# Kernel tuning notes

Measured on AMD Instinct MI355X. Metric: run time of the kernel, lower is better.

## Reference

```python
import jax, jax.numpy as jnp
import numpy as np

N = 8192
D_IN = 512
D_OUT = 256
ALPHA = 0.2
NEG = -9e15


def setup_inputs() -> dict:
    key = jax.random.key(0)
    k1, k2, k3, k4 = jax.random.split(key, 4)
    node = jax.random.normal(k1, (N, D_IN), dtype=jnp.float32)
    adj = jax.random.randint(k2, (N, N), 0, 2, dtype=jnp.int32)
    # xavier_uniform with gain=1.414
    gain = 1.414
    lim_w = gain * np.sqrt(6.0 / (D_IN + D_OUT))
    weight = jax.random.uniform(k3, (D_IN, D_OUT), minval=-lim_w, maxval=lim_w, dtype=jnp.float32)
    lim_a = gain * np.sqrt(6.0 / (2 * D_OUT + 1))
    a = jax.random.uniform(k4, (2 * D_OUT, 1), minval=-lim_a, maxval=lim_a, dtype=jnp.float32)
    bias = jnp.zeros((D_OUT,), dtype=jnp.float32)
    return {"node": node, "adj": adj, "weight": weight, "a": a, "bias": bias}


def reference(node, adj, weight, a, bias):
    # v: [N, D_OUT]
    v = node @ weight
    # per-node attention scalars: Q, K are [N, 1]
    Q = v @ a[:D_OUT, :]
    K = v @ a[D_OUT:, :]
    e = jax.nn.leaky_relu(Q + K.T, negative_slope=ALPHA)  # [N, N]
    attention = jnp.where(adj > 0, e, NEG)
    attention = jax.nn.softmax(attention, axis=1)
    # dropout is identity in eval mode (self.training == False)
    out = attention @ v  # [N, D_OUT]
    out = jax.nn.leaky_relu(out, negative_slope=ALPHA)
    # F.normalize(p=2, dim=1): x / max(||x||_2, 1e-12)
    norm = jnp.linalg.norm(out, axis=1, keepdims=True)
    out = out / jnp.maximum(norm, 1e-12)
    return out + bias
```

## Files before the change

### kernel.cpp

```cpp
#include <hip/hip_runtime.h>
#include <hip/hip_bf16.h>

#define N_NODES 8192
#define DIN     512
#define DOUT    256
#define ALPHA   0.2f
#define LOG2E   1.4426950408889634f

typedef __bf16 bf16x8 __attribute__((ext_vector_type(8)));
typedef __bf16 bf16x4 __attribute__((ext_vector_type(4)));
typedef float  f32x4  __attribute__((ext_vector_type(4)));
typedef int    i32x4  __attribute__((ext_vector_type(4)));
typedef unsigned u32x4 __attribute__((ext_vector_type(4)));

__global__ __launch_bounds__(256) void k_repack_w(const float* __restrict__ w,
                                                  bf16x8* __restrict__ wB,
                                                  unsigned* __restrict__ kmaxkey) {
    if (blockIdx.x == 0 && threadIdx.x == 0) *kmaxkey = 0u;
    int u = blockIdx.x * 256 + threadIdx.x;
    int lane = u & 63, t = u >> 6;
    int nt = t & 15, kt = t >> 4;
    int k0 = kt * 32 + (lane >> 4) * 8;
    int col = nt * 16 + (lane & 15);
    bf16x8 r;
#pragma unroll
    for (int i = 0; i < 8; ++i) r[i] = (__bf16)w[(size_t)(k0 + i) * DOUT + col];
    wB[u] = r;
}

__global__ __launch_bounds__(256) void k_gemm1f(const float* __restrict__ node,
                                                const bf16x8* __restrict__ wB,
                                                const float* __restrict__ a,
                                                bf16x8* __restrict__ vBo,
                                                float* __restrict__ Q, float* __restrict__ K,
                                                unsigned* __restrict__ kmaxkey) {
    __shared__ __bf16 vsh[32][260];
    __shared__ float qksh[32][2];
    int lane = threadIdx.x & 63, w = threadIdx.x >> 6;
    int r15 = lane & 15, g = lane >> 4;
    int nh = w & 1, rh = w >> 1;
    int rowbase = blockIdx.x * 32;
    int myrow = rowbase + rh * 16 + r15;
    const float* np = node + (size_t)myrow * DIN + g * 8;

    f32x4 acc[8];
#pragma unroll
    for (int j = 0; j < 8; ++j) acc[j] = (f32x4){0.f, 0.f, 0.f, 0.f};

    f32x4 c0 = *(const f32x4*)np;
    f32x4 c1 = *(const f32x4*)(np + 4);
    f32x4 c2 = *(const f32x4*)(np + 32);
    f32x4 c3 = *(const f32x4*)(np + 36);
    const bf16x8* wp = wB + (size_t)(nh * 8) * 64 + lane;
    bf16x8 fr0 = wp[0], fr1 = wp[64], fr2 = wp[128], fr3 = wp[192];
    bf16x8 fr4 = wp[256], fr5 = wp[320], fr6 = wp[384], fr7 = wp[448];

    for (int kt = 0; kt < 16; ++kt) {
        f32x4 u0 = c0, u1 = c1;
        c0 = c2; c1 = c3;
        if (kt + 2 < 16) {
            c2 = *(const f32x4*)(np + (kt + 2) * 32);
            c3 = *(const f32x4*)(np + (kt + 2) * 32 + 4);
        }
        bf16x8 f0 = fr0, f1 = fr1, f2 = fr2, f3 = fr3;
        bf16x8 f4 = fr4, f5 = fr5, f6 = fr6, f7 = fr7;
        if (kt + 1 < 16) {
            const bf16x8* wn = wB + ((size_t)(kt + 1) * 16 + nh * 8) * 64 + lane;
            fr0 = wn[0]; fr1 = wn[64]; fr2 = wn[128]; fr3 = wn[192];
            fr4 = wn[256]; fr5 = wn[320]; fr6 = wn[384]; fr7 = wn[448];
        }
        bf16x8 af;
#pragma unroll
        for (int i = 0; i < 4; ++i) { af[i] = (__bf16)u0[i]; af[i + 4] = (__bf16)u1[i]; }
        acc[0] = __builtin_amdgcn_mfma_f32_16x16x32_bf16(af, f0, acc[0], 0, 0, 0);
        acc[1] = __builtin_amdgcn_mfma_f32_16x16x32_bf16(af, f1, acc[1], 0, 0, 0);
        acc[2] = __builtin_amdgcn_mfma_f32_16x16x32_bf16(af, f2, acc[2], 0, 0, 0);
        acc[3] = __builtin_amdgcn_mfma_f32_16x16x32_bf16(af, f3, acc[3], 0, 0, 0);
        acc[4] = __builtin_amdgcn_mfma_f32_16x16x32_bf16(af, f4, acc[4], 0, 0, 0);
        acc[5] = __builtin_amdgcn_mfma_f32_16x16x32_bf16(af, f5, acc[5], 0, 0, 0);
        acc[6] = __builtin_amdgcn_mfma_f32_16x16x32_bf16(af, f6, acc[6], 0, 0, 0);
        acc[7] = __builtin_amdgcn_mfma_f32_16x16x32_bf16(af, f7, acc[7], 0, 0, 0);
    }

    float qp0 = 0.f, qp1 = 0.f, qp2 = 0.f, qp3 = 0.f;
    float kp0 = 0.f, kp1 = 0.f, kp2 = 0.f, kp3 = 0.f;
#pragma unroll
    for (int j = 0; j < 8; ++j) {
        int col = (nh * 8 + j) * 16 + r15;
        float a1 = a[col], a2 = a[DOUT + col];
        qp0 += acc[j][0] * a1; qp1 += acc[j][1] * a1;
        qp2 += acc[j][2] * a1; qp3 += acc[j][3] * a1;
        kp0 += acc[j][0] * a2; kp1 += acc[j][1] * a2;
        kp2 += acc[j][2] * a2; kp3 += acc[j][3] * a2;
    }
#pragma unroll
    for (int m = 1; m < 16; m <<= 1) {
        qp0 += __shfl_xor(qp0, m); qp1 += __shfl_xor(qp1, m);
        qp2 += __shfl_xor(qp2, m); qp3 += __shfl_xor(qp3, m);
        kp0 += __shfl_xor(kp0, m); kp1 += __shfl_xor(kp1, m);
        kp2 += __shfl_xor(kp2, m); kp3 += __shfl_xor(kp3, m);
    }

#pragma unroll
    for (int j = 0; j < 8; ++j)
#pragma unroll
        for (int r = 0; r < 4; ++r)
            vsh[rh * 16 + g * 4 + r][(nh * 8 + j) * 16 + r15] = (__bf16)acc[j][r];
    if (nh == 0 && r15 == 0) {
        int rl = rh * 16 + g * 4;
        qksh[rl + 0][0] = qp0; qksh[rl + 1][0] = qp1; qksh[rl + 2][0] = qp2; qksh[rl + 3][0] = qp3;
        qksh[rl + 0][1] = kp0; qksh[rl + 1][1] = kp1; qksh[rl + 2][1] = kp2; qksh[rl + 3][1] = kp3;
    }
    __syncthreads();
    if (nh == 1 && r15 == 0) {
        int rl = rh * 16 + g * 4;
        int rw = rowbase + rl;
        float q0 = qp0 + qksh[rl + 0][0], q1 = qp1 + qksh[rl + 1][0];
        float q2 = qp2 + qksh[rl + 2][0], q3 = qp3 + qksh[rl + 3][0];
        float k0 = kp0 + qksh[rl + 0][1], k1 = kp1 + qksh[rl + 1][1];
        float k2 = kp2 + qksh[rl + 2][1], k3 = kp3 + qksh[rl + 3][1];
        Q[rw + 0] = q0; Q[rw + 1] = q1; Q[rw + 2] = q2; Q[rw + 3] = q3;
        K[rw + 0] = k0; K[rw + 1] = k1; K[rw + 2] = k2; K[rw + 3] = k3;
        float km = fmaxf(fmaxf(k0, k1), fmaxf(k2, k3));
        unsigned bits = __float_as_uint(km);
        unsigned key = (bits & 0x80000000u) ? ~bits : (bits | 0x80000000u);
        atomicMax(kmaxkey, key);
    }
#pragma unroll
    for (int uu = 0; uu < 4; ++uu) {
        int nt = w * 4 + uu;
        bf16x8 t;
#pragma unroll
        for (int i = 0; i < 8; ++i) t[i] = vsh[g * 8 + i][nt * 16 + r15];
        vBo[((size_t)blockIdx.x * 16 + nt) * 64 + lane] = t;
    }
}

template<int JS>
__global__ __launch_bounds__(256, 2) void k_attn(const int* __restrict__ adj,
                                                 const bf16x8* __restrict__ vBg,
                                                 const float* __restrict__ Q,
                                                 const float* __restrict__ K,
                                                 const unsigned* __restrict__ kmaxkey,
                                                 __bf16* __restrict__ accB,
                                                 float* __restrict__ Sp) {
    constexpr int JR   = N_NODES / JS;
    constexpr int BIT  = JR / 32;
    constexpr int NG   = BIT / 4;
    constexpr int MSTR = BIT + 4;
    __shared__ float    Ks[JR];
    __shared__ unsigned Ms[64][MSTR];
    __shared__ bf16x8   pT[2][4][64];

    int bid = blockIdx.x;
    int rb = bid / JS, p = bid % JS;
    int lane = threadIdx.x & 63, w = threadIdx.x >> 6;
    int r15 = lane & 15, g = lane >> 4;
    int rowbase = rb * 64;
    int prow = rowbase + w * 16 + r15;
    int j0 = p * JR;

    for (int s = threadIdx.x * 4; s < JR; s += 1024)
        *(f32x4*)&Ks[s] = *(const f32x4*)&K[j0 + s];

    const int t = threadIdx.x;
    const int mrow = t >> 2, msub = t & 3;
    const int* abase = adj + (size_t)(rowbase + mrow) * N_NODES + j0;

#define ISSUE8(L, DC) { const int* src_ = abase + (DC) * 32;                     \
    _Pragma("unroll") for (int q = 0; q < 8; ++q) L[q] = *(const i32x4*)(src_ + q * 4); }
#define PACK32(L) ({ unsigned m_ = 0u;                                           \
    _Pragma("unroll") for (int q = 0; q < 8; ++q) {                              \
        m_ |= (L[q][0] != 0 ? 1u : 0u) << (q * 4 + 0);                           \
        m_ |= (L[q][1] != 0 ? 1u : 0u) << (q * 4 + 1);                           \
        m_ |= (L[q][2] != 0 ? 1u : 0u) << (q * 4 + 2);                           \
        m_ |= (L[q][3] != 0 ? 1u : 0u) << (q * 4 + 3); } m_; })

    i32x4 La[8];
    {
        i32x4 Lb[8];
        ISSUE8(La, msub)
        ISSUE8(Lb, 4 + msub)
        Ms[mrow][msub] = PACK32(La);
        Ms[mrow][4 + msub] = PACK32(Lb);
    }
    ISSUE8(La, 8 + msub)

    float qi = Q[prow];
    unsigned kk = *kmaxkey;
    unsigned kb = (kk & 0x80000000u) ? (kk ^ 0x80000000u) : ~kk;
    float kmax = __uint_as_float(kb);
    float t0 = qi + kmax;
    float c2 = fmaxf(t0, ALPHA * t0) * LOG2E;
    float qiL = qi * LOG2E;
    float A1 = qiL - c2;
    float A2 = ALPHA * qiL - c2;

    const bf16x8* vbp = vBg + ((size_t)(p * BIT) * 16 + w * 4) * 64 + lane;

    f32x4 acc[4][4];
#pragma unroll
    for (int m = 0; m < 4; ++m)
#pragma unroll
        for (int n = 0; n < 4; ++n) acc[m][n] = (f32x4){0.f, 0.f, 0.f, 0.f};
    float sl = 0.f;

    asm volatile("s_waitcnt lgkmcnt(0)" ::: "memory");
    __builtin_amdgcn_s_barrier();
    asm volatile("" ::: "memory");

    u32x4 Wc = *(const u32x4*)&Ms[w * 16 + r15][0];
    bf16x8 vS0 = vbp[0],    vS1 = vbp[64],   vS2 = vbp[128],  vS3 = vbp[192];
    bf16x8 vT0 = vbp[1024], vT1 = vbp[1088], vT2 = vbp[1152], vT3 = vbp[1216];

#define BODYM(W32, V0, V1, V2, V3, BUF, itv)                                    \
    {                                                                           \
        bf16x8 b0 = V0, b1 = V1, b2 = V2, b3 = V3;                              \
        if ((itv) + 2 < BIT) {                                                  \
            V0 = vbp[((itv) + 2) * 1024];       V1 = vbp[((itv) + 2) * 1024 + 64];  \
            V2 = vbp[((itv) + 2) * 1024 + 128]; V3 = vbp[((itv) + 2) * 1024 + 192]; \
        }                                                                       \
        f32x4 q0 = *(const f32x4*)&Ks[(itv) * 32 + g * 8];                      \
        f32x4 q1 = *(const f32x4*)&Ks[(itv) * 32 + g * 8 + 4];                  \
        unsigned wsh = (W32) >> (g * 8);                                        \
        bf16x8 af;                                                              \
        _Pragma("unroll")                                                       \
        for (int i = 0; i < 8; ++i) {                                           \
            float kj = (i < 4) ? q0[i] : q1[i - 4];                             \
            float f1 = __builtin_fmaf(kj, LOG2E, A1);                           \
            float f2 = __builtin_fmaf(kj, ALPHA * LOG2E, A2);                   \
            float pv = __builtin_amdgcn_exp2f(fmaxf(f1, f2));                   \
            pv = (wsh & (1u << i)) ? pv : 0.f;                                  \
            sl += pv;                                                           \
            af[i] = (__bf16)pv;                                                 \
        }                                                                       \
        pT[BUF][w][lane] = af;                                                  \
        asm volatile("s_waitcnt lgkmcnt(0)" ::: "memory");                      \
        __builtin_amdgcn_s_barrier();                                           \
        asm volatile("" ::: "memory");                                         \
        bf16x8 pa0 = pT[BUF][0][lane], pa1 = pT[BUF][1][lane];                  \
        bf16x8 pa2 = pT[BUF][2][lane], pa3 = pT[BUF][3][lane];                  \
        acc[0][0] = __builtin_amdgcn_mfma_f32_16x16x32_bf16(pa0, b0, acc[0][0], 0, 0, 0); \
        acc[0][1] = __builtin_amdgcn_mfma_f32_16x16x32_bf16(pa0, b1, acc[0][1], 0, 0, 0); \
        acc[0][2] = __builtin_amdgcn_mfma_f32_16x16x32_bf16(pa0, b2, acc[0][2], 0, 0, 0); \
        acc[0][3] = __builtin_amdgcn_mfma_f32_16x16x32_bf16(pa0, b3, acc[0][3], 0, 0, 0); \
        acc[1][0] = __builtin_amdgcn_mfma_f32_16x16x32_bf16(pa1, b0, acc[1][0], 0, 0, 0); \
        acc[1][1] = __builtin_amdgcn_mfma_f32_16x16x32_bf16(pa1, b1, acc[1][1], 0, 0, 0); \
        acc[1][2] = __builtin_amdgcn_mfma_f32_16x16x32_bf16(pa1, b2, acc[1][2], 0, 0, 0); \
        acc[1][3] = __builtin_amdgcn_mfma_f32_16x16x32_bf16(pa1, b3, acc[1][3], 0, 0, 0); \
        acc[2][0] = __builtin_amdgcn_mfma_f32_16x16x32_bf16(pa2, b0, acc[2][0], 0, 0, 0); \
        acc[2][1] = __builtin_amdgcn_mfma_f32_16x16x32_bf16(pa2, b1, acc[2][1], 0, 0, 0); \
        acc[2][2] = __builtin_amdgcn_mfma_f32_16x16x32_bf16(pa2, b2, acc[2][2], 0, 0, 0); \
        acc[2][3] = __builtin_amdgcn_mfma_f32_16x16x32_bf16(pa2, b3, acc[2][3], 0, 0, 0); \
        acc[3][0] = __builtin_amdgcn_mfma_f32_16x16x32_bf16(pa3, b0, acc[3][0], 0, 0, 0); \
        acc[3][1] = __builtin_amdgcn_mfma_f32_16x16x32_bf16(pa3, b1, acc[3][1], 0, 0, 0); \
        acc[3][2] = __builtin_amdgcn_mfma_f32_16x16x32_bf16(pa3, b2, acc[3][2], 0, 0, 0); \
        acc[3][3] = __builtin_amdgcn_mfma_f32_16x16x32_bf16(pa3, b3, acc[3][3], 0, 0, 0); \
    }

    for (int G = 0; G < NG; ++G) {
        const int it4 = G * 4;
        u32x4 Wn = Wc;
        if (G + 1 < NG) Wn = *(const u32x4*)&Ms[w * 16 + r15][it4 + 4];
        BODYM(Wc[0], vS0, vS1, vS2, vS3, 0, it4 + 0)
        BODYM(Wc[1], vT0, vT1, vT2, vT3, 1, it4 + 1)
        if (G + 2 < NG) {
            Ms[mrow][(G + 2) * 4 + msub] = PACK32(La);
            if (G + 3 < NG) ISSUE8(La, (G + 3) * 4 + msub)
        }
        BODYM(Wc[2], vS0, vS1, vS2, vS3, 0, it4 + 2)
        BODYM(Wc[3], vT0, vT1, vT2, vT3, 1, it4 + 3)
        Wc = Wn;
    }
#undef BODYM
#undef ISSUE8
#undef PACK32

    sl += __shfl_xor(sl, 16);
    sl += __shfl_xor(sl, 32);
    if (g == 0) Sp[(size_t)p * N_NODES + prow] = sl;

    __bf16* apb = accB + ((size_t)p * N_NODES + rowbase) * DOUT;
#pragma unroll
    for (int m = 0; m < 4; ++m)
#pragma unroll
        for (int r = 0; r < 4; ++r) {
            bf16x4 t2;
#pragma unroll
            for (int n = 0; n < 4; ++n) t2[n] = (__bf16)acc[m][n][r];
            *(bf16x4*)&apb[(size_t)(m * 16 + g * 4 + r) * DOUT + w * 64 + r15 * 4] = t2;
        }
}

template<int JS>
__global__ __launch_bounds__(256) void k_final(const __bf16* __restrict__ accB,
                                               const float* __restrict__ Sp,
                                               const float* __restrict__ bias,
                                               float* __restrict__ out) {
    int lane = threadIdx.x & 63, wv = threadIdx.x >> 6;
    int row = blockIdx.x * 4 + wv;
    float s = 0.f;
    f32x4 av = (f32x4){0.f, 0.f, 0.f, 0.f};
#pragma unroll
    for (int pp = 0; pp < JS; ++pp) {
        bf16x4 t = *(const bf16x4*)&accB[((size_t)pp * N_NODES + row) * DOUT + lane * 4];
#pragma unroll
        for (int j = 0; j < 4; ++j) av[j] += (float)t[j];
        s += Sp[(size_t)pp * N_NODES + row];
    }
    float inv = 1.0f / fmaxf(s, 1e-30f);
    f32x4 o;
#pragma unroll
    for (int j = 0; j < 4; ++j) {
        float x = av[j] * inv;
        o[j] = fmaxf(x, ALPHA * x);
    }
    float sq = o[0] * o[0] + o[1] * o[1] + o[2] * o[2] + o[3] * o[3];
#pragma unroll
    for (int m = 1; m < 64; m <<= 1) sq += __shfl_xor(sq, m);
    float innrm = 1.0f / fmaxf(sqrtf(sq), 1e-12f);
#pragma unroll
    for (int j = 0; j < 4; ++j) {
        int col = (lane >> 4) * 64 + j * 16 + (lane & 15);
        out[(size_t)row * DOUT + col] = o[j] * innrm + bias[col];
    }
}

extern "C" void kernel_launch(void* const* d_in, const int* in_sizes, int n_in,
                              void* d_out, int out_size, void* d_ws, size_t ws_size,
                              hipStream_t stream) {
    const float* node   = (const float*)d_in[0];
    const int*   adj    = (const int*)d_in[1];
    const float* weight = (const float*)d_in[2];
    const float* a      = (const float*)d_in[3];
    const float* bias   = (const float*)d_in[4];
    float* out = (float*)d_out;

    const size_t fixed  = 4522240;
    const size_t per_js = 32768 + (size_t)N_NODES * DOUT * 2;
    int js = (ws_size >= fixed + 8 * per_js) ? 8 : 4;

    char* ws = (char*)d_ws;
    bf16x8*   wB      = (bf16x8*)(ws);
    bf16x8*   vB      = (bf16x8*)(ws + 262144);
    float*    Q       = (float*)(ws + 4456448);
    float*    K       = (float*)(ws + 4489216);
    unsigned* kmaxkey = (unsigned*)(ws + 4521984);
    float*    Sp      = (float*)(ws + fixed);
    __bf16*   accB    = (__bf16*)(ws + fixed + (size_t)js * 32768);

    k_repack_w<<<dim3(64),  dim3(256), 0, stream>>>(weight, wB, kmaxkey);
    k_gemm1f  <<<dim3(256), dim3(256), 0, stream>>>(node, wB, a, vB, Q, K, kmaxkey);
    if (js == 8) {
        k_attn<8><<<dim3(128 * 8), dim3(256), 0, stream>>>(adj, vB, Q, K, kmaxkey, accB, Sp);
        k_final<8><<<dim3(2048), dim3(256), 0, stream>>>(accB, Sp, bias, out);
    } else {
        k_attn<4><<<dim3(128 * 4), dim3(256), 0, stream>>>(adj, vB, Q, K, kmaxkey, accB, Sp);
        k_final<4><<<dim3(2048), dim3(256), 0, stream>>>(accB, Sp, bias, out);
    }
}
```

Baseline: 122.1 us.

## Pack adjacency mask with wave ballots and coalesced row-contiguous loads

```diff
diff --git a/kernel.cpp b/kernel.cpp
--- a/kernel.cpp
+++ b/kernel.cpp
@@ -163,28 +163,37 @@
     for (int s = threadIdx.x * 4; s < JR; s += 1024)
         *(f32x4*)&Ks[s] = *(const f32x4*)&K[j0 + s];
 
-    const int t = threadIdx.x;
-    const int mrow = t >> 2, msub = t & 3;
-    const int* abase = adj + (size_t)(rowbase + mrow) * N_NODES + j0;
-
-#define ISSUE8(L, DC) { const int* src_ = abase + (DC) * 32;                     \
-    _Pragma("unroll") for (int q = 0; q < 8; ++q) L[q] = *(const i32x4*)(src_ + q * 4); }
-#define PACK32(L) ({ unsigned m_ = 0u;                                           \
-    _Pragma("unroll") for (int q = 0; q < 8; ++q) {                              \
-        m_ |= (L[q][0] != 0 ? 1u : 0u) << (q * 4 + 0);                           \
-        m_ |= (L[q][1] != 0 ? 1u : 0u) << (q * 4 + 1);                           \
-        m_ |= (L[q][2] != 0 ? 1u : 0u) << (q * 4 + 2);                           \
-        m_ |= (L[q][3] != 0 ? 1u : 0u) << (q * 4 + 3); } m_; })
+    const int hrow = w * 2 + (lane >> 5);
+    const int* abase = adj + (size_t)(rowbase + hrow) * N_NODES + j0 + (lane & 31) * 4;
+
+#define ISSUE8(L, GG) { _Pragma("unroll")                                        \
+    for (int q = 0; q < 8; ++q)                                                  \
+        L[q] = *(const i32x4*)(abase + (size_t)(q * 8) * N_NODES + (GG) * 128); }
+
+#define PACKB(L, GG) { _Pragma("unroll") for (int q = 0; q < 8; ++q) {           \
+    unsigned long long b0_ = __ballot(L[q][0] != 0);                             \
+    unsigned long long b1_ = __ballot(L[q][1] != 0);                             \
+    unsigned long long b2_ = __ballot(L[q][2] != 0);                             \
+    unsigned long long b3_ = __ballot(L[q][3] != 0);                             \
+    if ((lane & 31) == 0) {                                                      \
+        int hi_ = lane >> 5;                                                     \
+        u32x4 u_;                                                                \
+        u_[0] = hi_ ? (unsigned)(b0_ >> 32) : (unsigned)b0_;                     \
+        u_[1] = hi_ ? (unsigned)(b1_ >> 32) : (unsigned)b1_;                     \
+        u_[2] = hi_ ? (unsigned)(b2_ >> 32) : (unsigned)b2_;                     \
+        u_[3] = hi_ ? (unsigned)(b3_ >> 32) : (unsigned)b3_;                     \
+        *(u32x4*)&Ms[q * 8 + hrow][(GG) * 4] = u_;                               \
+    } } }
 
     i32x4 La[8];
     {
         i32x4 Lb[8];
-        ISSUE8(La, msub)
-        ISSUE8(Lb, 4 + msub)
-        Ms[mrow][msub] = PACK32(La);
-        Ms[mrow][4 + msub] = PACK32(Lb);
-    }
-    ISSUE8(La, 8 + msub)
+        ISSUE8(La, 0)
+        ISSUE8(Lb, 1)
+        PACKB(La, 0)
+        PACKB(Lb, 1)
+    }
+    ISSUE8(La, 2)
 
     float qi = Q[prow];
     unsigned kk = *kmaxkey;
@@ -209,11 +218,11 @@
     __builtin_amdgcn_s_barrier();
     asm volatile("" ::: "memory");
 
-    u32x4 Wc = *(const u32x4*)&Ms[w * 16 + r15][0];
+    u32x4 Uc = *(const u32x4*)&Ms[w * 16 + r15][0];
     bf16x8 vS0 = vbp[0],    vS1 = vbp[64],   vS2 = vbp[128],  vS3 = vbp[192];
     bf16x8 vT0 = vbp[1024], vT1 = vbp[1088], vT2 = vbp[1152], vT3 = vbp[1216];
 
-#define BODYM(W32, V0, V1, V2, V3, BUF, itv)                                    \
+#define BODYM(UU, S, V0, V1, V2, V3, BUF, itv)                                  \
     {                                                                           \
         bf16x8 b0 = V0, b1 = V1, b2 = V2, b3 = V3;                              \
         if ((itv) + 2 < BIT) {                                                  \
@@ -222,7 +231,9 @@
         }                                                                       \
         f32x4 q0 = *(const f32x4*)&Ks[(itv) * 32 + g * 8];                      \
         f32x4 q1 = *(const f32x4*)&Ks[(itv) * 32 + g * 8 + 4];                  \
-        unsigned wsh = (W32) >> (g * 8);                                        \
+        unsigned bsh = (S) * 8 + g * 2;                                         \
+        unsigned m0 = UU[0] >> bsh, m1 = UU[1] >> bsh;                          \
+        unsigned m2 = UU[2] >> bsh, m3 = UU[3] >> bsh;                          \
         bf16x8 af;                                                              \
         _Pragma("unroll")                                                       \
         for (int i = 0; i < 8; ++i) {                                           \
@@ -230,7 +241,8 @@
             float f1 = __builtin_fmaf(kj, LOG2E, A1);                           \
             float f2 = __builtin_fmaf(kj, ALPHA * LOG2E, A2);                   \
             float pv = __builtin_amdgcn_exp2f(fmaxf(f1, f2));                   \
-            pv = (wsh & (1u << i)) ? pv : 0.f;                                  \
+            unsigned mm_ = (i & 3) == 0 ? m0 : ((i & 3) == 1 ? m1 : ((i & 3) == 2 ? m2 : m3)); \
+            pv = (mm_ & (1u << (i >> 2))) ? pv : 0.f;                           \
             sl += pv;                                                           \
             af[i] = (__bf16)pv;                                                 \
         }                                                                       \
@@ -260,21 +272,21 @@
 
     for (int G = 0; G < NG; ++G) {
         const int it4 = G * 4;
-        u32x4 Wn = Wc;
-        if (G + 1 < NG) Wn = *(const u32x4*)&Ms[w * 16 + r15][it4 + 4];
-        BODYM(Wc[0], vS0, vS1, vS2, vS3, 0, it4 + 0)
-        BODYM(Wc[1], vT0, vT1, vT2, vT3, 1, it4 + 1)
+        u32x4 Un = Uc;
+        if (G + 1 < NG) Un = *(const u32x4*)&Ms[w * 16 + r15][it4 + 4];
+        BODYM(Uc, 0, vS0, vS1, vS2, vS3, 0, it4 + 0)
+        BODYM(Uc, 1, vT0, vT1, vT2, vT3, 1, it4 + 1)
         if (G + 2 < NG) {
-            Ms[mrow][(G + 2) * 4 + msub] = PACK32(La);
-            if (G + 3 < NG) ISSUE8(La, (G + 3) * 4 + msub)
+            PACKB(La, G + 2)
+            if (G + 3 < NG) ISSUE8(La, G + 3)
         }
-        BODYM(Wc[2], vS0, vS1, vS2, vS3, 0, it4 + 2)
-        BODYM(Wc[3], vT0, vT1, vT2, vT3, 1, it4 + 3)
-        Wc = Wn;
+        BODYM(Uc, 2, vS0, vS1, vS2, vS3, 0, it4 + 2)
+        BODYM(Uc, 3, vT0, vT1, vT2, vT3, 1, it4 + 3)
+        Uc = Un;
     }
 #undef BODYM
 #undef ISSUE8
-#undef PACK32
+#undef PACKB
 
     sl += __shfl_xor(sl, 16);
     sl += __shfl_xor(sl, 32);
```

Measured after the change: 113.0 us. -7.5%, faster.
